# Kernel optimization log

Measured on AMD Instinct MI355X. Metric: run time of the kernel, lower is better.

The kernel has to match this reference:

```python
import jax, jax.numpy as jnp
import numpy as np

N = 50000        # n_nodes
E = 1_600_000    # n_edges (avg degree 32)
IN = 128         # in_dim
H = 8            # num_heads
R = 16           # hidden_rank
D = 16           # out_dim (per head)
SCALE = float(np.sqrt(D))


def setup_inputs() -> dict:
    key = jax.random.key(0)
    k1, k2, k3, k4, k5, k6 = jax.random.split(key, 6)
    h = jax.random.normal(k1, (N, IN), jnp.float32)
    src = jax.random.randint(k2, (E,), 0, N, dtype=jnp.int32)
    dst = jax.random.randint(k3, (E,), 0, N, dtype=jnp.int32)
    s = 1.0 / np.sqrt(IN)  # kaiming-ish scale
    p = jax.random.normal(k4, (IN, H * R), jnp.float32) * s
    q = jax.random.normal(k5, (IN, H * R), jnp.float32) * s
    Wv = jax.random.normal(k6, (IN, H * D), jnp.float32) * s
    return {"h": h, "src": src, "dst": dst, "p": p, "q": q, "Wv": Wv}


def reference(h, src, dst, p, q, Wv):
    # global_attention_type == 'transform' -> atted = h
    K = (h @ q).reshape(N, H, R)   # K_h = atted @ _q
    Q = (h @ p).reshape(N, H, R)   # Q_h = h @ _p
    V = (h @ Wv).reshape(N, H, D)  # V_h = V(h), no bias
    # per-edge score: (K[src] * Q[dst]).sum(-1, keepdim), then scaled exp
    score = jnp.sum(K[src] * Q[dst], axis=-1, keepdims=True)   # [E, H, 1]
    score = jnp.exp(jnp.clip(score / SCALE, -5.0, 5.0))
    # scatter-sum into destination nodes
    wV = jax.ops.segment_sum(V[src] * score, dst, num_segments=N)  # [N, H, D]
    z = jax.ops.segment_sum(score, dst, num_segments=N)            # [N, H, 1]
    z = jnp.where(z == 0, jnp.float32(0.001), z)
    return wV / z
```

## Files before the change

kernel.cpp:

```cpp
#include <hip/hip_runtime.h>
#include <hip/hip_fp16.h>


#define HNODE 64
#define EPB   8192
#define BKT_SHIFT 7
#define BKT_CAP 5120

typedef _Float16 f16x8 __attribute__((ext_vector_type(8)));
typedef float    f32x4 __attribute__((ext_vector_type(4)));
typedef _Float16 hv2   __attribute__((ext_vector_type(2)));

__device__ __forceinline__ float fdot2(unsigned a, unsigned b, float c) {
#if __has_builtin(__builtin_amdgcn_fdot2)
    return __builtin_amdgcn_fdot2(__builtin_bit_cast(hv2, a),
                                  __builtin_bit_cast(hv2, b), c, false);
#else
    __half2 ah = *(__half2*)&a, bh = *(__half2*)&b;
    float2 af = __half22float2(ah), bf = __half22float2(bh);
    return c + af.x * bf.x + af.y * bf.y;
#endif
}

__device__ __forceinline__ float2 h2f(unsigned u) {
    __half2 hh = *(__half2*)&u;
    return __half22float2(hh);
}

__device__ __forceinline__ unsigned pack2(float a, float b) {
    __half2 hh = __floats2half2_rn(a, b);
    return *(unsigned*)&hh;
}

__global__ __launch_bounds__(256) void wt_convert_kernel(
    const float* __restrict__ Wq, const float* __restrict__ Wp,
    const float* __restrict__ Wv, __half* __restrict__ Wt)
{
    int o = blockIdx.x * 256 + threadIdx.x;
    int m = o >> 14, rem = o & 16383;
    int nn = rem >> 7, kk = rem & 127;
    const float* W = (m == 0) ? Wq : (m == 1) ? Wp : Wv;
    Wt[o] = __float2half(W[kk * 128 + nn]);
}

__global__ __launch_bounds__(256) void gemm_kqv_kernel(
    const float* __restrict__ h, const __half* __restrict__ Wt,
    unsigned* __restrict__ KV, __half* __restrict__ Q, int n)
{
    __shared__ __align__(16) _Float16 ws[128 * 136];

    const int t = threadIdx.x;
    const int wid = t >> 6, lane = t & 63;
    const int node0 = blockIdx.x * HNODE;
    const int mrow = lane & 15, quad = lane >> 4;

    const int row = node0 + wid * 16 + mrow;
    const bool rowvalid = (row < n);
    const int rowc = rowvalid ? row : (n - 1);

    f16x8 hfr[4];
    #pragma unroll
    for (int s = 0; s < 4; s++) {
        const float4* hp = (const float4*)(h + (size_t)rowc * 128 + quad * 8 + 32 * s);
        float4 f0 = hp[0], f1 = hp[1];
        f16x8 a;
        a[0] = (_Float16)f0.x; a[1] = (_Float16)f0.y;
        a[2] = (_Float16)f0.z; a[3] = (_Float16)f0.w;
        a[4] = (_Float16)f1.x; a[5] = (_Float16)f1.y;
        a[6] = (_Float16)f1.z; a[7] = (_Float16)f1.w;
        hfr[s] = a;
    }

    f32x4 acc[3][8];
    #pragma unroll
    for (int m = 0; m < 3; m++)
        #pragma unroll
        for (int ct = 0; ct < 8; ct++) acc[m][ct] = (f32x4){0.f, 0.f, 0.f, 0.f};

    #pragma unroll
    for (int m = 0; m < 3; m++) {
        __syncthreads();
        {
            const uint4* wg = (const uint4*)(Wt + (size_t)m * 16384);
            #pragma unroll
            for (int i = 0; i < 8; i++) {
                int idx = t * 8 + i;
                int r = idx >> 4, seg = idx & 15;
                *(uint4*)(ws + r * 136 + seg * 8) = wg[idx];
            }
        }
        __syncthreads();
        #pragma unroll
        for (int s = 0; s < 4; s++) {
            #pragma unroll
            for (int ct = 0; ct < 8; ct++) {
                f16x8 a = *(const f16x8*)(ws + (ct * 16 + mrow) * 136 + quad * 8 + 32 * s);
                acc[m][ct] = __builtin_amdgcn_mfma_f32_16x16x32_f16(a, hfr[s], acc[m][ct], 0, 0, 0);
            }
        }
    }

    if (rowvalid) {
        unsigned* kvrow = KV + (size_t)row * 128;
        __half*   qrow  = Q  + (size_t)row * 128;
        #pragma unroll
        for (int ct = 0; ct < 8; ct++) {
            int qd = ct * 4 + quad;
            uint4 ov;
            ov.x = pack2(acc[0][ct][0], acc[0][ct][1]);
            ov.y = pack2(acc[0][ct][2], acc[0][ct][3]);
            ov.z = pack2(acc[2][ct][0], acc[2][ct][1]);
            ov.w = pack2(acc[2][ct][2], acc[2][ct][3]);
            *(uint4*)(kvrow + 4 * qd) = ov;
            uint2 qv;
            qv.x = pack2(acc[1][ct][0], acc[1][ct][1]);
            qv.y = pack2(acc[1][ct][2], acc[1][ct][3]);
            *(uint2*)(qrow + 4 * qd) = qv;
        }
    }
}

__global__ __launch_bounds__(256) void bucket_scatter_kernel(
    const int* __restrict__ src, const int* __restrict__ dst,
    int* __restrict__ bucket_cursor, unsigned* __restrict__ ebuf, int E, int nbkt)
{
    __shared__ int cnt[512];
    __shared__ int start[512];
    int t = threadIdx.x;
    for (int i = t; i < nbkt; i += 256) cnt[i] = 0;
    __syncthreads();

    int4 sv[8], dv[8], rk[8];
    int base = blockIdx.x * EPB + t * 4;
    #pragma unroll
    for (int r = 0; r < 8; r++) {
        int i = base + r * 1024;
        if (i + 3 < E) {
            sv[r] = *(const int4*)(src + i);
            dv[r] = *(const int4*)(dst + i);
        } else {
            int ts[4], td[4];
            for (int k = 0; k < 4; k++) {
                int j = i + k;
                ts[k] = (j < E) ? src[j] : 0;
                td[k] = (j < E) ? dst[j] : -1;
            }
            sv[r] = make_int4(ts[0], ts[1], ts[2], ts[3]);
            dv[r] = make_int4(td[0], td[1], td[2], td[3]);
        }
        rk[r].x = (dv[r].x >= 0) ? atomicAdd(&cnt[dv[r].x >> BKT_SHIFT], 1) : 0;
        rk[r].y = (dv[r].y >= 0) ? atomicAdd(&cnt[dv[r].y >> BKT_SHIFT], 1) : 0;
        rk[r].z = (dv[r].z >= 0) ? atomicAdd(&cnt[dv[r].z >> BKT_SHIFT], 1) : 0;
        rk[r].w = (dv[r].w >= 0) ? atomicAdd(&cnt[dv[r].w >> BKT_SHIFT], 1) : 0;
    }
    __syncthreads();
    for (int i = t; i < nbkt; i += 256) {
        int c = cnt[i];
        start[i] = c ? atomicAdd(&bucket_cursor[i], c) : 0;
    }
    __syncthreads();
    #pragma unroll
    for (int r = 0; r < 8; r++) {
        int s, d, b, pos;
        d = dv[r].x; if (d >= 0) { s = sv[r].x; b = d >> BKT_SHIFT; pos = start[b] + rk[r].x; if (pos < BKT_CAP) ebuf[(size_t)b * BKT_CAP + pos] = ((unsigned)(d & 127) << 18) | (unsigned)s; }
        d = dv[r].y; if (d >= 0) { s = sv[r].y; b = d >> BKT_SHIFT; pos = start[b] + rk[r].y; if (pos < BKT_CAP) ebuf[(size_t)b * BKT_CAP + pos] = ((unsigned)(d & 127) << 18) | (unsigned)s; }
        d = dv[r].z; if (d >= 0) { s = sv[r].z; b = d >> BKT_SHIFT; pos = start[b] + rk[r].z; if (pos < BKT_CAP) ebuf[(size_t)b * BKT_CAP + pos] = ((unsigned)(d & 127) << 18) | (unsigned)s; }
        d = dv[r].w; if (d >= 0) { s = sv[r].w; b = d >> BKT_SHIFT; pos = start[b] + rk[r].w; if (pos < BKT_CAP) ebuf[(size_t)b * BKT_CAP + pos] = ((unsigned)(d & 127) << 18) | (unsigned)s; }
    }
}

__global__ __launch_bounds__(256) void fine_scatter_kernel(
    const unsigned* __restrict__ ebuf, const int* __restrict__ bucket_cursor,
    int2* __restrict__ offs, int* __restrict__ csr, int N, int nbkt)
{
    __shared__ int ldeg[128];
    __shared__ int lstart[128];
    int b = blockIdx.x, t = threadIdx.x;
    int node_base = b << BKT_SHIFT;
    int seg0 = b * BKT_CAP;
    int cnt = bucket_cursor[b];
    if (cnt > BKT_CAP) cnt = BKT_CAP;

    if (t < 128) ldeg[t] = 0;
    __syncthreads();

    unsigned pv[20];
    int rk[20];
    #pragma unroll
    for (int j = 0; j < 20; j++) {
        int i = t + j * 256;
        bool ok = (i < cnt);
        unsigned v = ok ? ebuf[seg0 + i] : 0u;
        pv[j] = v;
        rk[j] = ok ? atomicAdd(&ldeg[v >> 18], 1) : 0;
    }
    __syncthreads();

    int mydeg = (t < 128) ? ldeg[t] : 0;
    for (int off = 1; off < 128; off <<= 1) {
        int y = (t >= off && t < 128) ? ldeg[t - off] : 0;
        __syncthreads();
        if (t < 128) ldeg[t] += y;
        __syncthreads();
    }
    if (t < 128) {
        int gbeg = seg0 + ldeg[t] - mydeg;
        lstart[t] = gbeg;
        int node = node_base + t;
        if (node < N) offs[node] = make_int2(gbeg, gbeg + mydeg);
    }
    __syncthreads();

    #pragma unroll
    for (int j = 0; j < 20; j++) {
        int i = t + j * 256;
        if (i < cnt)
            csr[lstart[pv[j] >> 18] + rk[j]] = (int)(pv[j] & 0x3FFFFu);
    }
}

__global__ __launch_bounds__(256) void aggregate_kernel(
    const uint4* __restrict__ KV, const uint2* __restrict__ Qr,
    const int2* __restrict__ offs, const int* __restrict__ csr,
    float4* __restrict__ out, int n)
{
    int t = threadIdx.x;
    int node = blockIdx.x * 4 + (t >> 6);
    if (node >= n) return;
    int lane = t & 63;
    int l = lane & 31;
    int eh = lane >> 5;

    uint2 qq = Qr[(size_t)node * 32 + l];
    int2 be = offs[node];
    int beg = be.x, cnt = be.y - be.x;

    float4 accV = make_float4(0.f, 0.f, 0.f, 0.f);
    float accZ = 0.f;

    int chunkbase = 0;
    int myidx = (beg + lane < be.y) ? csr[beg + lane] : 0;

    uint4 kvA = make_uint4(0, 0, 0, 0), kvB = make_uint4(0, 0, 0, 0);
    if (cnt > 0) kvA = KV[(size_t)__shfl(myidx, eh, 64) * 32 + l];
    if (cnt > 2) kvB = KV[(size_t)__shfl(myidx, 2 + eh, 64) * 32 + l];

    for (int e = 0; e < cnt; e += 2) {
        uint4 nkv;
        bool more = (e + 4 < cnt);
        if (more) {
            int off = e + 4 - chunkbase;
            if (off == 64) {
                chunkbase += 64;
                myidx = (beg + chunkbase + lane < be.y) ? csr[beg + chunkbase + lane] : 0;
                off = 0;
            }
            nkv = KV[(size_t)__shfl(myidx, off + eh, 64) * 32 + l];
        }
        float p = fdot2(kvA.x, qq.x, fdot2(kvA.y, qq.y, 0.f));
        p += __shfl_xor(p, 1);
        p += __shfl_xor(p, 2);
        float x = fminf(fmaxf(p * 0.25f, -5.f), 5.f);
        float sc = (e + eh < cnt) ? __expf(x) : 0.f;
        accZ += sc;
        float2 va = h2f(kvA.z), vb = h2f(kvA.w);
        accV.x += sc * va.x; accV.y += sc * va.y;
        accV.z += sc * vb.x; accV.w += sc * vb.y;
        kvA = kvB;
        if (more) kvB = nkv;
    }

    accZ   += __shfl_xor(accZ, 32);
    accV.x += __shfl_xor(accV.x, 32);
    accV.y += __shfl_xor(accV.y, 32);
    accV.z += __shfl_xor(accV.z, 32);
    accV.w += __shfl_xor(accV.w, 32);

    if (lane < 32) {
        if (accZ == 0.f) accZ = 0.001f;
        float inv = 1.0f / accZ;
        out[(size_t)node * 32 + l] =
            make_float4(accV.x * inv, accV.y * inv, accV.z * inv, accV.w * inv);
    }
}


extern "C" void kernel_launch(void* const* d_in, const int* in_sizes, int n_in,
                              void* d_out, int out_size, void* d_ws, size_t ws_size,
                              hipStream_t stream)
{
    const float* h   = (const float*)d_in[0];
    const int*   src = (const int*)d_in[1];
    const int*   dst = (const int*)d_in[2];
    const float* p   = (const float*)d_in[3];
    const float* q   = (const float*)d_in[4];
    const float* wv  = (const float*)d_in[5];
    float* out = (float*)d_out;

    const int N = in_sizes[0] / 128;
    const int E = in_sizes[1];
    const int nbkt = (N + 127) >> BKT_SHIFT;

    unsigned* KV = (unsigned*)d_ws;
    __half* Qh   = (__half*)(KV + (size_t)N * 128);
    unsigned* ebuf = (unsigned*)(Qh + (size_t)N * 128);
    int* csr     = (int*)(ebuf + (size_t)nbkt * BKT_CAP);
    int2* offs   = (int2*)(csr + (size_t)nbkt * BKT_CAP);
    int* bucket_cursor = (int*)(offs + N);
    __half* Wt   = (__half*)(bucket_cursor + 512);

    (void)hipMemsetAsync(bucket_cursor, 0, 512 * sizeof(int), stream);

    wt_convert_kernel<<<192, 256, 0, stream>>>(q, p, wv, Wt);

    int nblk_e = (E + EPB - 1) / EPB;
    bucket_scatter_kernel<<<nblk_e, 256, 0, stream>>>(src, dst, bucket_cursor, ebuf, E, nbkt);

    gemm_kqv_kernel<<<(N + HNODE - 1) / HNODE, 256, 0, stream>>>(h, Wt, KV, Qh, N);

    fine_scatter_kernel<<<nbkt, 256, 0, stream>>>(ebuf, bucket_cursor, offs, csr, N, nbkt);

    aggregate_kernel<<<(N + 3) / 4, 256, 0, stream>>>(
        (const uint4*)KV, (const uint2*)Qh, offs, csr, (float4*)out, N);
}
```

Measured before the change: 253.0 us.

## Stage bucket and CSR scatters through shared memory for coalesced global writes

The bucket scatter kernel now sorts each block's edges by bucket in shared memory, using a local prefix scan over bucket counts. It then writes them to the global bucket buffer in sorted order, so consecutive threads write contiguous runs. The fine scatter kernel similarly builds the per-bucket CSR segment in shared memory and copies it out linearly. This trades random global stores for extra LDS traffic and barriers, and adds about 64KB of shared memory per block in the first kernel, which may reduce occupancy.

```diff
diff --git a/kernel.cpp b/kernel.cpp
--- a/kernel.cpp
+++ b/kernel.cpp
@@ -125,9 +125,14 @@
     int* __restrict__ bucket_cursor, unsigned* __restrict__ ebuf, int E, int nbkt)
 {
     __shared__ int cnt[512];
-    __shared__ int start[512];
+    __shared__ int lofs[512];
+    __shared__ int gstart[512];
+    __shared__ int ts[256];
+    __shared__ int tot_sh;
+    __shared__ unsigned long long sorted[EPB];
+
     int t = threadIdx.x;
-    for (int i = t; i < nbkt; i += 256) cnt[i] = 0;
+    for (int i = t; i < 512; i += 256) cnt[i] = 0;
     __syncthreads();
 
     int4 sv[8], dv[8], rk[8];
@@ -139,14 +144,14 @@
             sv[r] = *(const int4*)(src + i);
             dv[r] = *(const int4*)(dst + i);
         } else {
-            int ts[4], td[4];
+            int tsrc[4], tdst[4];
             for (int k = 0; k < 4; k++) {
                 int j = i + k;
-                ts[k] = (j < E) ? src[j] : 0;
-                td[k] = (j < E) ? dst[j] : -1;
+                tsrc[k] = (j < E) ? src[j] : 0;
+                tdst[k] = (j < E) ? dst[j] : -1;
             }
-            sv[r] = make_int4(ts[0], ts[1], ts[2], ts[3]);
-            dv[r] = make_int4(td[0], td[1], td[2], td[3]);
+            sv[r] = make_int4(tsrc[0], tsrc[1], tsrc[2], tsrc[3]);
+            dv[r] = make_int4(tdst[0], tdst[1], tdst[2], tdst[3]);
         }
         rk[r].x = (dv[r].x >= 0) ? atomicAdd(&cnt[dv[r].x >> BKT_SHIFT], 1) : 0;
         rk[r].y = (dv[r].y >= 0) ? atomicAdd(&cnt[dv[r].y >> BKT_SHIFT], 1) : 0;
@@ -154,18 +159,48 @@
         rk[r].w = (dv[r].w >= 0) ? atomicAdd(&cnt[dv[r].w >> BKT_SHIFT], 1) : 0;
     }
     __syncthreads();
-    for (int i = t; i < nbkt; i += 256) {
-        int c = cnt[i];
-        start[i] = c ? atomicAdd(&bucket_cursor[i], c) : 0;
-    }
-    __syncthreads();
+
+    int c0 = cnt[2 * t], c1 = cnt[2 * t + 1];
+    int ps = c0 + c1;
+    ts[t] = ps; __syncthreads();
+    for (int off = 1; off < 256; off <<= 1) {
+        int x = ts[t];
+        int y = (t >= off) ? ts[t - off] : 0;
+        __syncthreads();
+        ts[t] = x + y;
+        __syncthreads();
+    }
+    int pbase = ts[t] - ps;
+    lofs[2 * t] = pbase;
+    lofs[2 * t + 1] = pbase + c0;
+    if (t == 255) tot_sh = ts[255];
+    for (int i = t; i < nbkt; i += 256)
+        gstart[i] = cnt[i] ? atomicAdd(&bucket_cursor[i], cnt[i]) : 0;
+    __syncthreads();
+
     #pragma unroll
     for (int r = 0; r < 8; r++) {
-        int s, d, b, pos;
-        d = dv[r].x; if (d >= 0) { s = sv[r].x; b = d >> BKT_SHIFT; pos = start[b] + rk[r].x; if (pos < BKT_CAP) ebuf[(size_t)b * BKT_CAP + pos] = ((unsigned)(d & 127) << 18) | (unsigned)s; }
-        d = dv[r].y; if (d >= 0) { s = sv[r].y; b = d >> BKT_SHIFT; pos = start[b] + rk[r].y; if (pos < BKT_CAP) ebuf[(size_t)b * BKT_CAP + pos] = ((unsigned)(d & 127) << 18) | (unsigned)s; }
-        d = dv[r].z; if (d >= 0) { s = sv[r].z; b = d >> BKT_SHIFT; pos = start[b] + rk[r].z; if (pos < BKT_CAP) ebuf[(size_t)b * BKT_CAP + pos] = ((unsigned)(d & 127) << 18) | (unsigned)s; }
-        d = dv[r].w; if (d >= 0) { s = sv[r].w; b = d >> BKT_SHIFT; pos = start[b] + rk[r].w; if (pos < BKT_CAP) ebuf[(size_t)b * BKT_CAP + pos] = ((unsigned)(d & 127) << 18) | (unsigned)s; }
+        int s, d;
+        d = dv[r].x; if (d >= 0) { s = sv[r].x; sorted[lofs[d >> BKT_SHIFT] + rk[r].x] = ((unsigned long long)d << 18) | (unsigned)s; }
+        d = dv[r].y; if (d >= 0) { s = sv[r].y; sorted[lofs[d >> BKT_SHIFT] + rk[r].y] = ((unsigned long long)d << 18) | (unsigned)s; }
+        d = dv[r].z; if (d >= 0) { s = sv[r].z; sorted[lofs[d >> BKT_SHIFT] + rk[r].z] = ((unsigned long long)d << 18) | (unsigned)s; }
+        d = dv[r].w; if (d >= 0) { s = sv[r].w; sorted[lofs[d >> BKT_SHIFT] + rk[r].w] = ((unsigned long long)d << 18) | (unsigned)s; }
+    }
+    __syncthreads();
+
+    int tot = tot_sh;
+    #pragma unroll
+    for (int j = 0; j < 32; j++) {
+        int i = j * 256 + t;
+        if (i < tot) {
+            unsigned long long e = sorted[i];
+            int d = (int)(e >> 18);
+            int b = d >> BKT_SHIFT;
+            int pos = gstart[b] + (i - lofs[b]);
+            if (pos < BKT_CAP)
+                ebuf[(size_t)b * BKT_CAP + pos] =
+                    ((unsigned)(d & 127) << 18) | (unsigned)(e & 0x3FFFFu);
+        }
     }
 }
 
@@ -175,6 +210,7 @@
 {
     __shared__ int ldeg[128];
     __shared__ int lstart[128];
+    __shared__ int lcsr[BKT_CAP];
     int b = blockIdx.x, t = threadIdx.x;
     int node_base = b << BKT_SHIFT;
     int seg0 = b * BKT_CAP;
@@ -204,10 +240,10 @@
         __syncthreads();
     }
     if (t < 128) {
-        int gbeg = seg0 + ldeg[t] - mydeg;
-        lstart[t] = gbeg;
+        int lbeg = ldeg[t] - mydeg;
+        lstart[t] = lbeg;
         int node = node_base + t;
-        if (node < N) offs[node] = make_int2(gbeg, gbeg + mydeg);
+        if (node < N) offs[node] = make_int2(seg0 + lbeg, seg0 + lbeg + mydeg);
     }
     __syncthreads();
 
@@ -215,8 +251,12 @@
     for (int j = 0; j < 20; j++) {
         int i = t + j * 256;
         if (i < cnt)
-            csr[lstart[pv[j] >> 18] + rk[j]] = (int)(pv[j] & 0x3FFFFu);
-    }
+            lcsr[lstart[pv[j] >> 18] + rk[j]] = (int)(pv[j] & 0x3FFFFu);
+    }
+    __syncthreads();
+
+    for (int i = t; i < cnt; i += 256)
+        csr[seg0 + i] = lcsr[i];
 }
 
 __global__ __launch_bounds__(256) void aggregate_kernel(
```

Result: faster. 246.4 us (-2.6%).
